# Performance work log

Hardware: AMD Instinct MI355X
Metric: run time of the kernel (lower is better)

The kernel has to match this reference:

```python
import jax, jax.numpy as jnp
import numpy as np

DIM = 256
WH, WW = 7, 7
N = WH * WW
HEADS = 8
HEAD_DIM = DIM // HEADS
SCALE = HEAD_DIM ** -0.5
B_ = 4096
NW = 64  # windows per image; B_ % NW == 0


def _relative_position_index():
    coords = np.stack(np.meshgrid(np.arange(WH), np.arange(WW), indexing='ij'))  # (2,Wh,Ww)
    flat = coords.reshape(2, -1)  # (2,N)
    rel = flat[:, :, None] - flat[:, None, :]  # (2,N,N)
    rel = rel.transpose(1, 2, 0)  # (N,N,2)
    rel = rel + np.array([WH - 1, WW - 1])
    rel = rel * np.array([2 * WW - 1, 1])
    return rel.sum(-1).astype(np.int32)  # (N,N)


def setup_inputs() -> dict:
    key = jax.random.key(0)
    ks = jax.random.split(key, 7)
    num_rel = (2 * WH - 1) * (2 * WW - 1)
    return {
        'x': jax.random.normal(ks[0], (B_, N, DIM), jnp.float32),
        'mask': jax.random.normal(ks[1], (NW, N, N), jnp.float32),
        'qkv_w': jax.random.normal(ks[2], (DIM, 3 * DIM), jnp.float32) * 0.02,
        'qkv_b': jnp.zeros((3 * DIM,), jnp.float32),
        'proj_w': jax.random.normal(ks[3], (DIM, DIM), jnp.float32) * 0.02,
        'proj_b': jnp.zeros((DIM,), jnp.float32),
        'bias_table': jax.random.normal(ks[4], (num_rel, HEADS), jnp.float32) * 0.02,
        'rel_index': jnp.asarray(_relative_position_index()),
    }


def reference(x, mask, qkv_w, qkv_b, proj_w, proj_b, bias_table, rel_index):
    B, n, C = x.shape
    qkv = x @ qkv_w + qkv_b  # (B,N,3C)
    qkv = qkv.reshape(B, n, 3, HEADS, HEAD_DIM).transpose(2, 0, 3, 1, 4)
    q, k, v = qkv[0], qkv[1], qkv[2]  # (B,H,N,hd)
    attn = jnp.einsum('bhnd,bhmd->bhnm', q * SCALE, k)  # (B,H,N,N)
    rel_bias = bias_table[rel_index.reshape(-1)].reshape(n, n, HEADS)
    attn = attn + rel_bias.transpose(2, 0, 1)[None]  # (B,H,N,N)
    nW = mask.shape[0]
    attn = attn.reshape(-1, nW, HEADS, n, n) + mask[None, :, None]
    attn = attn.reshape(-1, HEADS, n, n)
    attn = jax.nn.softmax(attn, axis=-1)
    out = jnp.einsum('bhnm,bhmd->bhnd', attn, v)  # (B,H,N,hd)
    out = out.transpose(0, 2, 1, 3).reshape(B, n, C)
    return out @ proj_w + proj_b
```

## Files before the change

### kernel.cpp

```cpp
#include <hip/hip_runtime.h>
#include <hip/hip_bf16.h>


#define NTOK 49
static constexpr float SCALE_Q = 0.17677669529663687f;

using bf16   = __bf16;
using bf16x4 = __attribute__((ext_vector_type(4))) __bf16;
using bf16x8 = __attribute__((ext_vector_type(8))) __bf16;
using short4v = __attribute__((ext_vector_type(4))) short;
using f32x4  = __attribute__((ext_vector_type(4))) float;

#define WT_QKV_OFF 0
#define WT_PROJ_OFF (768 * 256 * 2)
#define SB_OFF (WT_PROJ_OFF + 256 * 256 * 2)
#define SM_OFF (SB_OFF + 8 * 4096 * 4)
#define WS_NEEDED (SM_OFF + (size_t)64 * 4096 * 4)

static __device__ __forceinline__ f32x4 mfma16(bf16x4 a, bf16x4 b, f32x4 c) {
#if __has_builtin(__builtin_amdgcn_mfma_f32_16x16x16_bf16)
    return __builtin_amdgcn_mfma_f32_16x16x16_bf16(a, b, c, 0, 0, 0);
#elif __has_builtin(__builtin_amdgcn_mfma_f32_16x16x16bf16_1k)
    return __builtin_amdgcn_mfma_f32_16x16x16bf16_1k(
        __builtin_bit_cast(short4v, a), __builtin_bit_cast(short4v, b), c, 0, 0, 0);
#elif __has_builtin(__builtin_amdgcn_mfma_f32_16x16x16_bf16_1k)
    return __builtin_amdgcn_mfma_f32_16x16x16_bf16_1k(
        __builtin_bit_cast(short4v, a), __builtin_bit_cast(short4v, b), c, 0, 0, 0);
#else
    asm volatile("v_mfma_f32_16x16x16_bf16 %0, %1, %2, %0\n\t"
                 "s_nop 7\n\ts_nop 7\n\ts_nop 1"
                 : "+v"(c) : "v"(a), "v"(b));
    return c;
#endif
}

__global__ void prep_wqkv(const float* __restrict__ qkv_w, bf16* __restrict__ wt) {
    int idx = blockIdx.x * 256 + threadIdx.x;
    if (idx >= 768 * 256) return;
    int n = idx >> 8, k = idx & 255;
    float v = qkv_w[k * 768 + n];
    if (n < 256) v *= SCALE_Q;
    wt[idx] = (bf16)v;
}
__global__ void prep_wproj(const float* __restrict__ proj_w, bf16* __restrict__ wt) {
    int idx = blockIdx.x * 256 + threadIdx.x;
    if (idx >= 256 * 256) return;
    int n = idx >> 8, k = idx & 255;
    wt[idx] = (bf16)proj_w[k * 256 + n];
}
__global__ void prep_sb(const float* __restrict__ bias_table, const int* __restrict__ rel_index,
                        float* __restrict__ sb) {
    int idx = blockIdx.x * 256 + threadIdx.x;
    if (idx >= 8 * 4096) return;
    int r    = idx & 3;
    int lane = (idx >> 2) & 63;
    int qp   = (idx >> 8) & 15;
    int h    = idx >> 12;
    int kt = qp >> 2, qt = qp & 3;
    int i = qt * 16 + (lane & 15);
    int j = kt * 16 + (lane >> 4) * 4 + r;
    float v;
    if (j >= NTOK)      v = -1e30f;
    else if (i >= NTOK) v = 0.0f;
    else v = bias_table[rel_index[i * 49 + j] * 8 + h];
    sb[idx] = v;
}
__global__ void prep_sm(const float* __restrict__ mask, float* __restrict__ sm) {
    int idx = blockIdx.x * 256 + threadIdx.x;
    if (idx >= 64 * 4096) return;
    int r    = idx & 3;
    int lane = (idx >> 2) & 63;
    int qp   = (idx >> 8) & 15;
    int w    = idx >> 12;
    int kt = qp >> 2, qt = qp & 3;
    int i = qt * 16 + (lane & 15);
    int j = kt * 16 + (lane >> 4) * 4 + r;
    sm[idx] = (i < NTOK && j < NTOK) ? mask[(w * 49 + i) * 49 + j] : 0.0f;
}

__global__ __launch_bounds__(512, 2) void fused_attn(
    const float* __restrict__ x,
    const float* __restrict__ qkv_b,
    const float* __restrict__ proj_b,
    const bf16* __restrict__ wt_qkv,
    const bf16* __restrict__ wt_proj,
    const float* __restrict__ sb,
    const float* __restrict__ sm,
    float* __restrict__ out)
{
    __shared__ char smem[49152];
    char* xs  = smem;
    char* smL = smem + 32768;
    const int b    = blockIdx.x;
    const int tid  = threadIdx.x;
    const int lane = tid & 63;
    const int h    = tid >> 6;
    const int c    = lane & 15;
    const int g    = lane >> 4;

    {
        const float* xb = x + (size_t)b * (NTOK * 256);
        #pragma unroll
        for (int it = 0; it < 8; ++it) {
            int idx = it * 512 + tid;
            int row = idx >> 6, c4 = idx & 63;
            float4 v = make_float4(0.f, 0.f, 0.f, 0.f);
            if (row < NTOK) v = ((const float4*)xb)[row * 64 + c4];
            bf16x4 o;
            o[0] = (bf16)v.x; o[1] = (bf16)v.y; o[2] = (bf16)v.z; o[3] = (bf16)v.w;
            *(bf16x4*)(xs + row * 512 + ((c4 * 8) ^ ((row & 7) << 4))) = o;
        }
        const float4* smw = (const float4*)(sm + (size_t)(b & 63) * 4096);
        #pragma unroll
        for (int t = 0; t < 2; ++t) {
            int off = t * 512 + tid;
            *(float4*)(smL + off * 16) = smw[off];
        }
    }
    __syncthreads();

    bf16x4 iden;
    #pragma unroll
    for (int j = 0; j < 4; ++j) iden[j] = (bf16)((4 * g + j == c) ? 1.0f : 0.0f);

    bf16x4 qf[4][2];
    bf16x4 kf[4][2];
    bf16x4 vf[2][4];

    {
        f32x4 acc[6][4];
        #pragma unroll
        for (int ni = 0; ni < 6; ++ni)
            #pragma unroll
            for (int mi = 0; mi < 4; ++mi)
                acc[ni][mi] = (f32x4){0.f, 0.f, 0.f, 0.f};

        __builtin_amdgcn_s_setprio(1);
        #pragma unroll
        for (int kk = 0; kk < 8; ++kk) {
            bf16x8 a[4];
            #pragma unroll
            for (int mi = 0; mi < 4; ++mi) {
                int row = mi * 16 + c;
                a[mi] = *(const bf16x8*)(xs + row * 512 + ((kk * 64 + g * 16) ^ ((row & 7) << 4)));
            }
            #pragma unroll
            for (int ni = 0; ni < 6; ++ni) {
                int ncol = (ni >> 1) * 256 + h * 32 + (ni & 1) * 16 + c;
                bf16x8 bfr = *(const bf16x8*)(wt_qkv + ncol * 256 + kk * 32 + g * 8);
                #pragma unroll
                for (int mi = 0; mi < 4; ++mi)
                    acc[ni][mi] = __builtin_amdgcn_mfma_f32_16x16x32_bf16(a[mi], bfr, acc[ni][mi], 0, 0, 0);
            }
        }
        __builtin_amdgcn_s_setprio(0);

        #pragma unroll
        for (int ni = 0; ni < 6; ++ni) {
            int col = (ni >> 1) * 256 + h * 32 + (ni & 1) * 16 + c;
            float bias = qkv_b[col];
            if (ni < 2) bias *= SCALE_Q;
            #pragma unroll
            for (int mi = 0; mi < 4; ++mi) {
                bf16x4 in;
                #pragma unroll
                for (int r = 0; r < 4; ++r) in[r] = (bf16)(acc[ni][mi][r] + bias);
                if (ni < 4) {
                    f32x4 t = mfma16(in, iden, (f32x4){0.f, 0.f, 0.f, 0.f});
                    bf16x4 o;
                    #pragma unroll
                    for (int r = 0; r < 4; ++r) o[r] = (bf16)t[r];
                    if (ni < 2) qf[mi][ni] = o;
                    else        kf[mi][ni - 2] = o;
                } else {
                    vf[ni - 4][mi] = in;
                }
            }
        }
    }
    __syncthreads();

    const float* sbh = sb + (size_t)h * 4096;
    #pragma unroll
    for (int qt = 0; qt < 4; ++qt) {
        f32x4 sbv[4], smv[4];
        #pragma unroll
        for (int kt = 0; kt < 4; ++kt)
            sbv[kt] = *(const f32x4*)(sbh + (kt * 4 + qt) * 256 + lane * 4);
        #pragma unroll
        for (int kt = 0; kt < 4; ++kt)
            smv[kt] = *(const f32x4*)(smL + ((kt * 4 + qt) * 64 + lane) * 16);

        f32x4 sT[4];
        __builtin_amdgcn_s_setprio(1);
        #pragma unroll
        for (int kt = 0; kt < 4; ++kt) {
            sT[kt] = (f32x4){0.f, 0.f, 0.f, 0.f};
            sT[kt] = mfma16(kf[kt][0], qf[qt][0], sT[kt]);
            sT[kt] = mfma16(kf[kt][1], qf[qt][1], sT[kt]);
        }
        __builtin_amdgcn_s_setprio(0);
        #pragma unroll
        for (int kt = 0; kt < 4; ++kt)
            #pragma unroll
            for (int r = 0; r < 4; ++r)
                sT[kt][r] += sbv[kt][r] + smv[kt][r];
        float m = sT[0][0];
        #pragma unroll
        for (int kt = 0; kt < 4; ++kt)
            #pragma unroll
            for (int r = 0; r < 4; ++r) m = fmaxf(m, sT[kt][r]);
        m = fmaxf(m, __shfl_xor(m, 16));
        m = fmaxf(m, __shfl_xor(m, 32));
        float sum = 0.f;
        #pragma unroll
        for (int kt = 0; kt < 4; ++kt)
            #pragma unroll
            for (int r = 0; r < 4; ++r) {
                float e = __expf(sT[kt][r] - m);
                sT[kt][r] = e;
                sum += e;
            }
        sum += __shfl_xor(sum, 16);
        sum += __shfl_xor(sum, 32);
        float rs = 1.f / sum;
        bf16x4 pB[4];
        #pragma unroll
        for (int kt = 0; kt < 4; ++kt)
            #pragma unroll
            for (int r = 0; r < 4; ++r) pB[kt][r] = (bf16)(sT[kt][r] * rs);
        __builtin_amdgcn_s_setprio(1);
        #pragma unroll
        for (int dt = 0; dt < 2; ++dt) {
            f32x4 oT = (f32x4){0.f, 0.f, 0.f, 0.f};
            #pragma unroll
            for (int kt = 0; kt < 4; ++kt)
                oT = mfma16(vf[dt][kt], pB[kt], oT);
            int row = qt * 16 + c;
            int cbyte = h * 64 + dt * 32 + g * 8;
            bf16x4 o;
            #pragma unroll
            for (int r = 0; r < 4; ++r) o[r] = (bf16)oT[r];
            *(bf16x4*)(xs + row * 512 + (cbyte ^ ((row & 7) << 4))) = o;
        }
        __builtin_amdgcn_s_setprio(0);
    }
    __syncthreads();

    {
        f32x4 po[2][4];
        #pragma unroll
        for (int ni = 0; ni < 2; ++ni)
            #pragma unroll
            for (int mi = 0; mi < 4; ++mi)
                po[ni][mi] = (f32x4){0.f, 0.f, 0.f, 0.f};

        __builtin_amdgcn_s_setprio(1);
        #pragma unroll
        for (int kk = 0; kk < 8; ++kk) {
            bf16x8 a[4];
            #pragma unroll
            for (int mi = 0; mi < 4; ++mi) {
                int row = mi * 16 + c;
                a[mi] = *(const bf16x8*)(xs + row * 512 + ((kk * 64 + g * 16) ^ ((row & 7) << 4)));
            }
            #pragma unroll
            for (int ni = 0; ni < 2; ++ni) {
                int col = h * 32 + ni * 16 + c;
                bf16x8 bw = *(const bf16x8*)(wt_proj + col * 256 + kk * 32 + g * 8);
                #pragma unroll
                for (int mi = 0; mi < 4; ++mi)
                    po[ni][mi] = __builtin_amdgcn_mfma_f32_16x16x32_bf16(a[mi], bw, po[ni][mi], 0, 0, 0);
            }
        }
        __builtin_amdgcn_s_setprio(0);
        float* outb = out + (size_t)b * (NTOK * 256);
        #pragma unroll
        for (int ni = 0; ni < 2; ++ni) {
            int col = h * 32 + ni * 16 + c;
            float pb = proj_b[col];
            #pragma unroll
            for (int mi = 0; mi < 4; ++mi) {
                #pragma unroll
                for (int r = 0; r < 4; ++r) {
                    int row = mi * 16 + g * 4 + r;
                    if (row < NTOK) outb[row * 256 + col] = po[ni][mi][r] + pb;
                }
            }
        }
    }
}

extern "C" void kernel_launch(void* const* d_in, const int* in_sizes, int n_in,
                              void* d_out, int out_size, void* d_ws, size_t ws_size,
                              hipStream_t stream) {
    const float* x          = (const float*)d_in[0];
    const float* mask       = (const float*)d_in[1];
    const float* qkv_w      = (const float*)d_in[2];
    const float* qkv_b      = (const float*)d_in[3];
    const float* proj_w     = (const float*)d_in[4];
    const float* proj_b     = (const float*)d_in[5];
    const float* bias_table = (const float*)d_in[6];
    const int*   rel_index  = (const int*)d_in[7];
    float* out = (float*)d_out;

    if (ws_size < WS_NEEDED) return;

    char* ws = (char*)d_ws;
    bf16*  wt_qkv  = (bf16*)(ws + WT_QKV_OFF);
    bf16*  wt_proj = (bf16*)(ws + WT_PROJ_OFF);
    float* sbp     = (float*)(ws + SB_OFF);
    float* smp     = (float*)(ws + SM_OFF);

    prep_wqkv <<<768, 256, 0, stream>>>(qkv_w, wt_qkv);
    prep_wproj<<<256, 256, 0, stream>>>(proj_w, wt_proj);
    prep_sb   <<<128, 256, 0, stream>>>(bias_table, rel_index, sbp);
    prep_sm   <<<1024, 256, 0, stream>>>(mask, smp);

    fused_attn<<<4096, 512, 0, stream>>>(x, qkv_b, proj_b, wt_qkv, wt_proj, sbp, smp, out);
}
```

Before: 424.5 us.

## Split QKV GEMM into QK and V passes, drop mask LDS staging

```diff
diff --git a/kernel.cpp b/kernel.cpp
--- a/kernel.cpp
+++ b/kernel.cpp
@@ -88,9 +88,7 @@
     const float* __restrict__ sm,
     float* __restrict__ out)
 {
-    __shared__ char smem[49152];
-    char* xs  = smem;
-    char* smL = smem + 32768;
+    __shared__ char xs[32768];
     const int b    = blockIdx.x;
     const int tid  = threadIdx.x;
     const int lane = tid & 63;
@@ -100,21 +98,22 @@
 
     {
         const float* xb = x + (size_t)b * (NTOK * 256);
+        float4 xr[8];
         #pragma unroll
         for (int it = 0; it < 8; ++it) {
             int idx = it * 512 + tid;
             int row = idx >> 6, c4 = idx & 63;
-            float4 v = make_float4(0.f, 0.f, 0.f, 0.f);
-            if (row < NTOK) v = ((const float4*)xb)[row * 64 + c4];
+            xr[it] = make_float4(0.f, 0.f, 0.f, 0.f);
+            if (row < NTOK) xr[it] = ((const float4*)xb)[row * 64 + c4];
+        }
+        #pragma unroll
+        for (int it = 0; it < 8; ++it) {
+            int idx = it * 512 + tid;
+            int row = idx >> 6, c4 = idx & 63;
             bf16x4 o;
-            o[0] = (bf16)v.x; o[1] = (bf16)v.y; o[2] = (bf16)v.z; o[3] = (bf16)v.w;
+            o[0] = (bf16)xr[it].x; o[1] = (bf16)xr[it].y;
+            o[2] = (bf16)xr[it].z; o[3] = (bf16)xr[it].w;
             *(bf16x4*)(xs + row * 512 + ((c4 * 8) ^ ((row & 7) << 4))) = o;
-        }
-        const float4* smw = (const float4*)(sm + (size_t)(b & 63) * 4096);
-        #pragma unroll
-        for (int t = 0; t < 2; ++t) {
-            int off = t * 512 + tid;
-            *(float4*)(smL + off * 16) = smw[off];
         }
     }
     __syncthreads();
@@ -128,16 +127,21 @@
     bf16x4 vf[2][4];
 
     {
-        f32x4 acc[6][4];
-        #pragma unroll
-        for (int ni = 0; ni < 6; ++ni)
+        f32x4 acc[4][4];
+        #pragma unroll
+        for (int ni = 0; ni < 4; ++ni)
             #pragma unroll
             for (int mi = 0; mi < 4; ++mi)
                 acc[ni][mi] = (f32x4){0.f, 0.f, 0.f, 0.f};
 
-        __builtin_amdgcn_s_setprio(1);
         #pragma unroll
         for (int kk = 0; kk < 8; ++kk) {
+            bf16x8 bb[4];
+            #pragma unroll
+            for (int ni = 0; ni < 4; ++ni) {
+                int ncol = (ni >> 1) * 256 + h * 32 + (ni & 1) * 16 + c;
+                bb[ni] = *(const bf16x8*)(wt_qkv + ncol * 256 + kk * 32 + g * 8);
+            }
             bf16x8 a[4];
             #pragma unroll
             for (int mi = 0; mi < 4; ++mi) {
@@ -145,18 +149,13 @@
                 a[mi] = *(const bf16x8*)(xs + row * 512 + ((kk * 64 + g * 16) ^ ((row & 7) << 4)));
             }
             #pragma unroll
-            for (int ni = 0; ni < 6; ++ni) {
-                int ncol = (ni >> 1) * 256 + h * 32 + (ni & 1) * 16 + c;
-                bf16x8 bfr = *(const bf16x8*)(wt_qkv + ncol * 256 + kk * 32 + g * 8);
+            for (int ni = 0; ni < 4; ++ni)
                 #pragma unroll
                 for (int mi = 0; mi < 4; ++mi)
-                    acc[ni][mi] = __builtin_amdgcn_mfma_f32_16x16x32_bf16(a[mi], bfr, acc[ni][mi], 0, 0, 0);
-            }
-        }
-        __builtin_amdgcn_s_setprio(0);
-
-        #pragma unroll
-        for (int ni = 0; ni < 6; ++ni) {
+                    acc[ni][mi] = __builtin_amdgcn_mfma_f32_16x16x32_bf16(a[mi], bb[ni], acc[ni][mi], 0, 0, 0);
+        }
+        #pragma unroll
+        for (int ni = 0; ni < 4; ++ni) {
             int col = (ni >> 1) * 256 + h * 32 + (ni & 1) * 16 + c;
             float bias = qkv_b[col];
             if (ni < 2) bias *= SCALE_Q;
@@ -165,22 +164,57 @@
                 bf16x4 in;
                 #pragma unroll
                 for (int r = 0; r < 4; ++r) in[r] = (bf16)(acc[ni][mi][r] + bias);
-                if (ni < 4) {
-                    f32x4 t = mfma16(in, iden, (f32x4){0.f, 0.f, 0.f, 0.f});
-                    bf16x4 o;
-                    #pragma unroll
-                    for (int r = 0; r < 4; ++r) o[r] = (bf16)t[r];
-                    if (ni < 2) qf[mi][ni] = o;
-                    else        kf[mi][ni - 2] = o;
-                } else {
-                    vf[ni - 4][mi] = in;
-                }
-            }
+                f32x4 t = mfma16(in, iden, (f32x4){0.f, 0.f, 0.f, 0.f});
+                bf16x4 o;
+                #pragma unroll
+                for (int r = 0; r < 4; ++r) o[r] = (bf16)t[r];
+                if (ni < 2) qf[mi][ni] = o;
+                else        kf[mi][ni - 2] = o;
+            }
+        }
+    }
+
+    {
+        f32x4 acc[2][4];
+        #pragma unroll
+        for (int dt = 0; dt < 2; ++dt)
+            #pragma unroll
+            for (int mi = 0; mi < 4; ++mi)
+                acc[dt][mi] = (f32x4){0.f, 0.f, 0.f, 0.f};
+
+        #pragma unroll
+        for (int kk = 0; kk < 8; ++kk) {
+            bf16x8 bv[2];
+            #pragma unroll
+            for (int dt = 0; dt < 2; ++dt) {
+                int ncol = 512 + h * 32 + dt * 16 + c;
+                bv[dt] = *(const bf16x8*)(wt_qkv + ncol * 256 + kk * 32 + g * 8);
+            }
+            bf16x8 a[4];
+            #pragma unroll
+            for (int mi = 0; mi < 4; ++mi) {
+                int row = mi * 16 + c;
+                a[mi] = *(const bf16x8*)(xs + row * 512 + ((kk * 64 + g * 16) ^ ((row & 7) << 4)));
+            }
+            #pragma unroll
+            for (int dt = 0; dt < 2; ++dt)
+                #pragma unroll
+                for (int mi = 0; mi < 4; ++mi)
+                    acc[dt][mi] = __builtin_amdgcn_mfma_f32_16x16x32_bf16(a[mi], bv[dt], acc[dt][mi], 0, 0, 0);
+        }
+        #pragma unroll
+        for (int dt = 0; dt < 2; ++dt) {
+            float vb = qkv_b[512 + h * 32 + dt * 16 + c];
+            #pragma unroll
+            for (int kt = 0; kt < 4; ++kt)
+                #pragma unroll
+                for (int r = 0; r < 4; ++r) vf[dt][kt][r] = (bf16)(acc[dt][kt][r] + vb);
         }
     }
     __syncthreads();
 
     const float* sbh = sb + (size_t)h * 4096;
+    const float* smw = sm + (size_t)(b & 63) * 4096;
     #pragma unroll
     for (int qt = 0; qt < 4; ++qt) {
         f32x4 sbv[4], smv[4];
@@ -189,7 +223,7 @@
             sbv[kt] = *(const f32x4*)(sbh + (kt * 4 + qt) * 256 + lane * 4);
         #pragma unroll
         for (int kt = 0; kt < 4; ++kt)
-            smv[kt] = *(const f32x4*)(smL + ((kt * 4 + qt) * 64 + lane) * 16);
+            smv[kt] = *(const f32x4*)(smw + (kt * 4 + qt) * 256 + lane * 4);
 
         f32x4 sT[4];
         __builtin_amdgcn_s_setprio(1);
@@ -255,9 +289,14 @@
             for (int mi = 0; mi < 4; ++mi)
                 po[ni][mi] = (f32x4){0.f, 0.f, 0.f, 0.f};
 
-        __builtin_amdgcn_s_setprio(1);
         #pragma unroll
         for (int kk = 0; kk < 8; ++kk) {
+            bf16x8 bw[2];
+            #pragma unroll
+            for (int ni = 0; ni < 2; ++ni) {
+                int col = h * 32 + ni * 16 + c;
+                bw[ni] = *(const bf16x8*)(wt_proj + col * 256 + kk * 32 + g * 8);
+            }
             bf16x8 a[4];
             #pragma unroll
             for (int mi = 0; mi < 4; ++mi) {
@@ -265,15 +304,11 @@
                 a[mi] = *(const bf16x8*)(xs + row * 512 + ((kk * 64 + g * 16) ^ ((row & 7) << 4)));
             }
             #pragma unroll
-            for (int ni = 0; ni < 2; ++ni) {
-                int col = h * 32 + ni * 16 + c;
-                bf16x8 bw = *(const bf16x8*)(wt_proj + col * 256 + kk * 32 + g * 8);
+            for (int ni = 0; ni < 2; ++ni)
                 #pragma unroll
                 for (int mi = 0; mi < 4; ++mi)
-                    po[ni][mi] = __builtin_amdgcn_mfma_f32_16x16x32_bf16(a[mi], bw, po[ni][mi], 0, 0, 0);
-            }
-        }
-        __builtin_amdgcn_s_setprio(0);
+                    po[ni][mi] = __builtin_amdgcn_mfma_f32_16x16x32_bf16(a[mi], bw[ni], po[ni][mi], 0, 0, 0);
+        }
         float* outb = out + (size_t)b * (NTOK * 256);
         #pragma unroll
         for (int ni = 0; ni < 2; ++ni) {
```

After: 394.3 us. 1.08x faster.
